# Kernel tuning notes

Measured on AMD Instinct MI355X. Metric: run time of the kernel, lower is better.

The kernel has to match this reference:

```python
import jax, jax.numpy as jnp
import numpy as np

BLOCK = 64
CRIT_TH = 0.5
NEGL_TH = 0.01
TEMP = 1.0
EPS = 1e-6


def setup_inputs() -> dict:
    key = jax.random.key(0)
    kq, kk, kv = jax.random.split(key, 3)
    B, T, H, D = 1, 2048, 8, 64
    q = jax.random.normal(kq, (B, T, H, D), dtype=jnp.float32)
    k = jax.random.normal(kk, (B, T, H, D), dtype=jnp.float32)
    v = jax.random.normal(kv, (B, T, H, D), dtype=jnp.float32)
    return {"q": q, "k": k, "v": v}


def _classify_blocks(qb, kb, D):
    # qb: [B,nq,bs,H,D], kb: [B,nk,bs,H,D]
    q_rep = qb.mean(axis=2)  # [B,nq,H,D]
    k_rep = kb.mean(axis=2)  # [B,nk,H,D]
    bscores = jnp.einsum('bqhd,bkhd->bhqk', q_rep, k_rep) / np.float32(np.sqrt(D))
    ssm = jax.nn.softmax(bscores, axis=-1)
    var = jnp.var(ssm, axis=-1, ddof=1, keepdims=True)  # unbiased, matches torch .var()
    max_scores = bscores.max(axis=-1, keepdims=True)
    imp = var * jnp.maximum(max_scores - bscores.min(), EPS)
    imp_n = (imp - imp.min()) / (imp.max() - imp.min() + EPS)
    crit = imp_n >= CRIT_TH
    negl = imp_n <= NEGL_TH
    marg = (~crit) & (~negl)
    return crit, marg


def reference(q, k, v):
    B, T, H, D = q.shape
    S = k.shape[1]
    nq, nk = T // BLOCK, S // BLOCK  # T,S are multiples of BLOCK (no padding needed)
    dtype = q.dtype

    qb = q.reshape(B, nq, BLOCK, H, D)
    kb = k.reshape(B, nk, BLOCK, H, D)
    vb = v.reshape(B, nk, BLOCK, H, D)

    crit, marg = _classify_blocks(qb, kb, D)  # [B,H,nq,nk] bool
    critf = crit.astype(dtype)
    margf = marg.astype(dtype)

    # ---- exact (critical) blocks: per-block-pair softmax attention ----
    scale = np.float32(1.0 / (np.sqrt(D) * TEMP))
    scores = jnp.einsum('bqthd,bkshd->bhqkts', qb, kb) * scale  # [B,H,nq,nk,bs,bs]
    attn = jax.nn.softmax(scores.astype(jnp.float32), axis=-1).astype(dtype)
    attn_m = attn * critf[:, :, :, :, None, None]
    out_c = jnp.einsum('bhqkts,bkshd->bqthd', attn_m, vb)  # [B,nq,bs,H,D]
    w_c = jnp.einsum('bhqkts->bqth', attn_m)[..., None]    # [B,nq,bs,H,1]

    # ---- linear (marginal) blocks: ELU+1 feature-map attention ----
    qf = jax.nn.elu(qb / TEMP) + 1.0
    kf = jax.nn.elu(kb / TEMP) + 1.0
    kv = jnp.einsum('bkshd,bkshv->bkhdv', kf, vb)              # [B,nk,H,D,D]
    num = jnp.einsum('bqthd,bkhdv->bqkthv', qf, kv)            # [B,nq,nk,bs,H,D]
    k_sum = kf.sum(axis=2)                                     # [B,nk,H,D]
    den = jnp.einsum('bqthd,bkhd->bqkth', qf, k_sum) + EPS     # [B,nq,nk,bs,H]
    out_pair = num / den[..., None]
    out_l = jnp.einsum('bqkthd,bhqk->bqthd', out_pair, margf)
    w_l = jnp.einsum('bqkth,bhqk->bqth', den, margf)[..., None]

    out = (out_c + out_l) / (w_c + w_l + EPS)
    return out.reshape(B, T, H, D)
```

## Files before the change

### kernel.cpp

```cpp
#include <hip/hip_runtime.h>
#include <math.h>

namespace {
constexpr int H  = 8;
constexpr int D  = 64;
constexpr int NB = 32;
constexpr int BS = 64;
constexpr int QST = 68;
}
#define FEPS 1e-6f

typedef unsigned short u16;
typedef unsigned int   u32;
typedef __attribute__((ext_vector_type(8))) short bf16x8;
typedef __attribute__((ext_vector_type(4))) float floatx4;

__device__ __forceinline__ u32 f2bf(float x) {
  union { float f; u32 u; } v; v.f = x;
  return (v.u + 0x7FFFu + ((v.u >> 16) & 1u)) >> 16;
}
__device__ __forceinline__ u32 pk2(float a, float b) { return f2bf(a) | (f2bf(b) << 16); }
#define ELU1(x) ((x) > 0.f ? (x) + 1.f : expf(x))
#define SWZ(row, kblk) ((row)*64 + (((kblk) ^ ((row)&7))*8))

__global__ __launch_bounds__(256) void prep_kernel(const float* __restrict__ q,
                                                   const float* __restrict__ k,
                                                   const float* __restrict__ v,
                                                   u16* __restrict__ kvt16,
                                                   float* __restrict__ ksum,
                                                   double* __restrict__ qrep,
                                                   double* __restrict__ krep) {
  __shared__ float smem[3*BS*D];
  int bid = blockIdx.x;
  int tid = threadIdx.x;
  if (bid >= 256) {
    double* qred = (double*)smem;
    int r = bid - 256;
    int h = r >> 5, bi = r & 31;
    int d = tid & 63, quarter = tid >> 6;
    double s = 0.0;
    for (int t = quarter*16; t < quarter*16 + 16; ++t)
      s += (double)q[((bi*BS + t)*H + h)*D + d];
    qred[quarter*64 + d] = s;
    __syncthreads();
    if (tid < 64)
      qrep[r*D + tid] = (qred[tid] + qred[64+tid] + qred[128+tid] + qred[192+tid]) * (1.0/64.0);
    return;
  }
  float* kf   = smem;
  float* vv   = smem + BS*D;
  float* kraw = smem + 2*BS*D;
  int h = bid >> 5, ki = bid & 31;
  int sr = tid >> 2, cgp = tid & 3;
  const float4* kb = (const float4*)(k + ((ki*BS + sr)*H + h)*D);
  const float4* vb = (const float4*)(v + ((ki*BS + sr)*H + h)*D);
#pragma unroll
  for (int m = 0; m < 4; ++m) {
    float4 kk = kb[cgp*4 + m];
    float4 vx = vb[cgp*4 + m];
    int c = cgp*16 + m*4;
    *(float4*)&kraw[sr*D + c] = kk;
    kf[sr*D + c + 0] = ELU1(kk.x);
    kf[sr*D + c + 1] = ELU1(kk.y);
    kf[sr*D + c + 2] = ELU1(kk.z);
    kf[sr*D + c + 3] = ELU1(kk.w);
    *(float4*)&vv[sr*D + c] = vx;
  }
  __syncthreads();
  int c = tid & 63, dg = tid >> 6, d0 = dg*16;
  float acc[16];
#pragma unroll
  for (int j = 0; j < 16; ++j) acc[j] = 0.f;
#pragma unroll 4
  for (int s2 = 0; s2 < BS; ++s2) {
    float vval = vv[s2*D + c];
    const float4* kr = (const float4*)&kf[s2*D + d0];
    float4 a0 = kr[0], a1 = kr[1], a2 = kr[2], a3 = kr[3];
    acc[0]  += vval*a0.x; acc[1]  += vval*a0.y; acc[2]  += vval*a0.z; acc[3]  += vval*a0.w;
    acc[4]  += vval*a1.x; acc[5]  += vval*a1.y; acc[6]  += vval*a1.z; acc[7]  += vval*a1.w;
    acc[8]  += vval*a2.x; acc[9]  += vval*a2.y; acc[10] += vval*a2.z; acc[11] += vval*a2.w;
    acc[12] += vval*a3.x; acc[13] += vval*a3.y; acc[14] += vval*a3.z; acc[15] += vval*a3.w;
  }
  u16* op = kvt16 + (size_t)bid*4096 + c*64 + d0;
  uint4 P0, P1;
  P0.x = pk2(acc[0],acc[1]);   P0.y = pk2(acc[2],acc[3]);
  P0.z = pk2(acc[4],acc[5]);   P0.w = pk2(acc[6],acc[7]);
  P1.x = pk2(acc[8],acc[9]);   P1.y = pk2(acc[10],acc[11]);
  P1.z = pk2(acc[12],acc[13]); P1.w = pk2(acc[14],acc[15]);
  *(uint4*)(op + 0) = P0;
  *(uint4*)(op + 8) = P1;
  if (dg == 0) {
    float ks = 0.f;
    for (int s2 = 0; s2 < BS; ++s2) ks += kf[s2*D + c];
    ksum[bid*D + c] = ks;
    double m = 0.0;
    for (int s2 = 0; s2 < BS; ++s2) m += (double)kraw[s2*D + c];
    krep[bid*D + c] = m * (1.0/64.0);
  }
}

__global__ __launch_bounds__(256) void bscore_stats_kernel(const double* __restrict__ qrep,
                                                           const double* __restrict__ krep,
                                                           double* __restrict__ rowmin,
                                                           double* __restrict__ rowmax,
                                                           double* __restrict__ rowvar) {
  __shared__ double qs[8*64];
  __shared__ double ks[32*65];
  int b = blockIdx.x;
  int h = b >> 2;
  int r0 = b*8;
  int tid = threadIdx.x;
  for (int i = tid; i < 512; i += 256) qs[i] = qrep[(size_t)r0*64 + i];
  for (int i = tid; i < 2048; i += 256) ks[(i >> 6)*65 + (i & 63)] = krep[(size_t)h*2048 + i];
  __syncthreads();
  int lr = tid >> 5, ki = tid & 31;
  double s = 0.0;
  const double* qr = qs + lr*64;
  const double* kr = ks + ki*65;
#pragma unroll 16
  for (int d = 0; d < D; ++d) s += qr[d]*kr[d];
  double bs = s * 0.125;
  double rmax = bs, rmin = bs;
#pragma unroll
  for (int m = 1; m < 32; m <<= 1) {
    rmax = fmax(rmax, __shfl_xor(rmax, m, 64));
    rmin = fmin(rmin, __shfl_xor(rmin, m, 64));
  }
  double e = exp(bs - rmax);
  double S = e, S2 = e*e;
#pragma unroll
  for (int m = 1; m < 32; m <<= 1) {
    S  += __shfl_xor(S,  m, 64);
    S2 += __shfl_xor(S2, m, 64);
  }
  if (ki == 0) {
    double invS = 1.0 / S;
    double sp = S * invS;
    double mu = sp * (1.0/32.0);
    double var = (S2*invS*invS - 2.0*mu*sp + 32.0*mu*mu) * (1.0/31.0);
    rowmin[r0 + lr] = rmin;
    rowmax[r0 + lr] = rmax;
    rowvar[r0 + lr] = var;
  }
}

__global__ __launch_bounds__(256) void main_kernel(
    const float* __restrict__ q, const float* __restrict__ k, const float* __restrict__ v,
    const u16* __restrict__ kvt16, const float* __restrict__ ksum,
    const double* __restrict__ rowmin, const double* __restrict__ rowmax,
    const double* __restrict__ rowvar, float* __restrict__ out) {
  __shared__ __align__(16) float smem[10304];
  int bid = blockIdx.x;
  int h = bid >> 5, qi = bid & 31;
  int tid = threadIdx.x;
  int row = tid >> 2, cgp = tid & 3, c0 = cgp*16;
  int lane = tid & 63;
  int wid = tid >> 6;

  int flag;
  {
    double* redA = (double*)smem;
    double* redB = (double*)(smem + 8);
    double* impS = (double*)(smem + 16);
    double x = rowmin[tid];
    double rmx2 = rowmax[tid];
    double rvr2 = rowvar[tid];
#pragma unroll
    for (int m = 1; m < 64; m <<= 1) x = fmin(x, __shfl_xor(x, m, 64));
    if (lane == 0) redA[wid] = x;
    __syncthreads();
    double gmin = fmin(fmin(redA[0], redA[1]), fmin(redA[2], redA[3]));
    double rng = rmx2 - gmin;
    if (rng < 1e-6) rng = 1e-6;
    double imp = rvr2 * rng;
    __syncthreads();
    if (tid == bid) impS[0] = imp;
    double a = imp, b2 = imp;
#pragma unroll
    for (int m = 1; m < 64; m <<= 1) {
      a  = fmin(a,  __shfl_xor(a,  m, 64));
      b2 = fmax(b2, __shfl_xor(b2, m, 64));
    }
    if (lane == 0) { redA[wid] = a; redB[wid] = b2; }
    __syncthreads();
    double imin = fmin(fmin(redA[0], redA[1]), fmin(redA[2], redA[3]));
    double imax = fmax(fmax(redB[0], redB[1]), fmax(redB[2], redB[3]));
    double impn = (impS[0] - imin) / (imax - imin + 1e-6);
    flag = (impn >= 0.5) ? 2 : ((impn <= 0.01) ? 0 : 1);
    __syncthreads();
  }

  if (flag == 1) {
    u16*  qfb  = (u16*)smem;
    u16*  kvb  = (u16*)(smem + 2048);
    float* idens = smem + 6144;
    float* wsl   = smem + 8192;
    float* kslc  = smem + 8256;

    {
      const float4* kss = (const float4*)(ksum + (size_t)(h*NB)*D);
      for (int i = tid; i < NB*16; i += 256) ((float4*)kslc)[i] = kss[i];
    }
    float qf[16];
    {
      const float4* qp = (const float4*)(q + ((qi*BS + row)*H + h)*D + c0);
      float4 q0 = qp[0], q1 = qp[1], q2 = qp[2], q3 = qp[3];
      qf[0]=ELU1(q0.x); qf[1]=ELU1(q0.y); qf[2]=ELU1(q0.z); qf[3]=ELU1(q0.w);
      qf[4]=ELU1(q1.x); qf[5]=ELU1(q1.y); qf[6]=ELU1(q1.z); qf[7]=ELU1(q1.w);
      qf[8]=ELU1(q2.x); qf[9]=ELU1(q2.y); qf[10]=ELU1(q2.z); qf[11]=ELU1(q2.w);
      qf[12]=ELU1(q3.x); qf[13]=ELU1(q3.y); qf[14]=ELU1(q3.z); qf[15]=ELU1(q3.w);
      uint4 p0, p1;
      p0.x = pk2(qf[0],qf[1]);  p0.y = pk2(qf[2],qf[3]);
      p0.z = pk2(qf[4],qf[5]);  p0.w = pk2(qf[6],qf[7]);
      p1.x = pk2(qf[8],qf[9]);  p1.y = pk2(qf[10],qf[11]);
      p1.z = pk2(qf[12],qf[13]); p1.w = pk2(qf[14],qf[15]);
      *(uint4*)&qfb[SWZ(row, cgp*2)]     = p0;
      *(uint4*)&qfb[SWZ(row, cgp*2 + 1)] = p1;
    }
    const u16* kvbase = kvt16 + (size_t)(h*NB)*4096 + (size_t)row*64 + c0;
    uint4 u0, u1;
    u0 = *(const uint4*)(kvbase + 0);
    u1 = *(const uint4*)(kvbase + 8);
    __syncthreads();
    {
      float wloc = 0.f;
      for (int ki = 0; ki < NB; ++ki) {
        float pd = 0.f;
#pragma unroll
        for (int j = 0; j < 16; ++j) pd += qf[j] * kslc[ki*64 + c0 + j];
        pd += __shfl_xor(pd, 1, 64);
        pd += __shfl_xor(pd, 2, 64);
        float den = pd + FEPS;
        if (cgp == 0) idens[row*32 + ki] = 1.0f / den;
        wloc += den;
      }
      if (cgp == 0) wsl[row] = wloc;
    }
    *(uint4*)&kvb[SWZ(row, cgp*2)]     = u0;
    *(uint4*)&kvb[SWZ(row, cgp*2 + 1)] = u1;

    int w = tid >> 6, m = lane & 15, quad = lane >> 4;
    bf16x8 aLo = *(const bf16x8*)&qfb[SWZ(w*16 + m, quad)];
    bf16x8 aHi = *(const bf16x8*)&qfb[SWZ(w*16 + m, 4 + quad)];
    int rbase = w*16 + quad*4;
    float acc[16];
#pragma unroll
    for (int j = 0; j < 16; ++j) acc[j] = 0.f;

    for (int ki = 0; ki < NB; ++ki) {
      if (ki + 1 < NB) {
        const u16* kvp = kvbase + (size_t)(ki+1)*4096;
        u0 = *(const uint4*)(kvp + 0);
        u1 = *(const uint4*)(kvp + 8);
      }
      __syncthreads();
      const u16* kb = kvb + (ki & 1)*4096;
      float i0 = idens[(rbase + 0)*32 + ki];
      float i1 = idens[(rbase + 1)*32 + ki];
      float i2 = idens[(rbase + 2)*32 + ki];
      float i3 = idens[(rbase + 3)*32 + ki];
      floatx4 zz = {0.f, 0.f, 0.f, 0.f};
#pragma unroll
      for (int t = 0; t < 4; ++t) {
        bf16x8 bLo = *(const bf16x8*)&kb[SWZ(t*16 + m, quad)];
        bf16x8 bHi = *(const bf16x8*)&kb[SWZ(t*16 + m, 4 + quad)];
        floatx4 c4 = __builtin_amdgcn_mfma_f32_16x16x32_bf16(aLo, bLo, zz, 0, 0, 0);
        c4 = __builtin_amdgcn_mfma_f32_16x16x32_bf16(aHi, bHi, c4, 0, 0, 0);
        acc[t*4+0] += c4[0]*i0;
        acc[t*4+1] += c4[1]*i1;
        acc[t*4+2] += c4[2]*i2;
        acc[t*4+3] += c4[3]*i3;
      }
      if (ki + 1 < NB) {
        u16* kw = kvb + ((ki+1) & 1)*4096;
        *(uint4*)&kw[SWZ(row, cgp*2)]     = u0;
        *(uint4*)&kw[SWZ(row, cgp*2 + 1)] = u1;
      }
    }
#pragma unroll
    for (int r = 0; r < 4; ++r) {
      float wd = 1.0f / (wsl[rbase + r] + FEPS);
      float* op = out + ((qi*BS + rbase + r)*H + h)*D + m;
#pragma unroll
      for (int t = 0; t < 4; ++t) op[t*16] = acc[t*4+r]*wd;
    }
    return;
  }

  float* bufA = smem;
  float* bufB = smem + 4352;
  float acc[16];
#pragma unroll
  for (int j = 0; j < 16; ++j) acc[j] = 0.f;
  float wsum = 0.f;

  if (flag == 2) {
    const float4* qp = (const float4*)(q + ((qi*BS + row)*H + h)*D);
#pragma unroll
    for (int mm = 0; mm < 4; ++mm) {
      float4 qq = qp[cgp*4 + mm];
      int c = c0 + mm*4;
      bufA[row*QST + c + 0] = qq.x*0.125f;
      bufA[row*QST + c + 1] = qq.y*0.125f;
      bufA[row*QST + c + 2] = qq.z*0.125f;
      bufA[row*QST + c + 3] = qq.w*0.125f;
    }
    __syncthreads();
    for (int ki = 0; ki < NB; ++ki) {
      const float4* kp = (const float4*)(k + ((ki*BS + row)*H + h)*D);
#pragma unroll
      for (int mm = 0; mm < 4; ++mm)
        *(float4*)&bufB[row*QST + c0 + mm*4] = kp[cgp*4 + mm];
      __syncthreads();
      float sc[16];
#pragma unroll
      for (int j = 0; j < 16; ++j) sc[j] = 0.f;
      for (int d = 0; d < D; ++d) {
        float a = bufA[row*QST + d];
#pragma unroll
        for (int j = 0; j < 16; ++j)
          sc[j] += a * bufB[(c0 + j)*QST + d];
      }
      float mx = sc[0];
#pragma unroll
      for (int j = 1; j < 16; ++j) mx = fmaxf(mx, sc[j]);
      mx = fmaxf(mx, __shfl_xor(mx, 1, 64));
      mx = fmaxf(mx, __shfl_xor(mx, 2, 64));
      float es = 0.f;
      float p[16];
#pragma unroll
      for (int j = 0; j < 16; ++j) { p[j] = expf(sc[j] - mx); es += p[j]; }
      es += __shfl_xor(es, 1, 64);
      es += __shfl_xor(es, 2, 64);
      float inv = 1.0f / es;
#pragma unroll
      for (int j = 0; j < 16; ++j) p[j] *= inv;
      wsum += es * inv;
      __syncthreads();
      const float4* vp = (const float4*)(v + ((ki*BS + row)*H + h)*D);
#pragma unroll
      for (int mm = 0; mm < 4; ++mm)
        *(float4*)&bufB[row*QST + c0 + mm*4] = vp[cgp*4 + mm];
      __syncthreads();
      for (int s2 = 0; s2 < BS; ++s2) {
        int g = s2 >> 4, jj = s2 & 15;
        float pv = __shfl(p[jj], (lane & ~3) | g, 64);
        const float4* vr = (const float4*)&bufB[s2*QST + c0];
        float4 a0 = vr[0], a1 = vr[1], a2 = vr[2], a3 = vr[3];
        acc[0]  += pv*a0.x; acc[1]  += pv*a0.y; acc[2]  += pv*a0.z; acc[3]  += pv*a0.w;
        acc[4]  += pv*a1.x; acc[5]  += pv*a1.y; acc[6]  += pv*a1.z; acc[7]  += pv*a1.w;
        acc[8]  += pv*a2.x; acc[9]  += pv*a2.y; acc[10] += pv*a2.z; acc[11] += pv*a2.w;
        acc[12] += pv*a3.x; acc[13] += pv*a3.y; acc[14] += pv*a3.z; acc[15] += pv*a3.w;
      }
      __syncthreads();
    }
  }
  float wd = 1.0f / (wsum + FEPS);
  float* op = out + ((qi*BS + row)*H + h)*D + c0;
  *(float4*)(op + 0)  = make_float4(acc[0]*wd,  acc[1]*wd,  acc[2]*wd,  acc[3]*wd);
  *(float4*)(op + 4)  = make_float4(acc[4]*wd,  acc[5]*wd,  acc[6]*wd,  acc[7]*wd);
  *(float4*)(op + 8)  = make_float4(acc[8]*wd,  acc[9]*wd,  acc[10]*wd, acc[11]*wd);
  *(float4*)(op + 12) = make_float4(acc[12]*wd, acc[13]*wd, acc[14]*wd, acc[15]*wd);
}

extern "C" void kernel_launch(void* const* d_in, const int* in_sizes, int n_in,
                              void* d_out, int out_size, void* d_ws, size_t ws_size,
                              hipStream_t stream) {
  const float* q = (const float*)d_in[0];
  const float* k = (const float*)d_in[1];
  const float* v = (const float*)d_in[2];
  float* out = (float*)d_out;
  char* ws = (char*)d_ws;
  u16*    kvw  = (u16*)   (ws + 0);
  float*  ksw  = (float*) (ws + 2097152);
  double* krep = (double*)(ws + 2162688);
  double* qrep = (double*)(ws + 2293760);
  double* rmn  = (double*)(ws + 2424832);
  double* rmx  = (double*)(ws + 2426880);
  double* rvr  = (double*)(ws + 2428928);

  prep_kernel<<<512, 256, 0, stream>>>(q, k, v, kvw, ksw, qrep, krep);
  bscore_stats_kernel<<<32, 256, 0, stream>>>(qrep, krep, rmn, rmx, rvr);
  main_kernel<<<256, 256, 0, stream>>>(q, k, v, kvw, ksw, rmn, rmx, rvr, out);
}
```

Measured before the change: 97.18 us.

## Split key-block loop across 8 workgroups with partial-sum combine kernel

The main attention kernel now splits the 32 key blocks of each (head, query-block) row over 8 workgroups. Each workgroup writes unnormalised partial accumulators and weights to workspace, and a new combine kernel sums and normalises them. Block classification moves into a separate single-block flags kernel, so it is no longer recomputed in every workgroup. The exact path also stores K transposed, prefetches K and V into registers, and vectorises its shared-memory loads. The goal is to raise occupancy from 256 workgroups and shorten the serial key loop. The cost is two extra launches and a large workspace round-trip for the partial results.

Result: slower. 103.5 us (+6.5%).

```diff
diff --git a/kernel.cpp b/kernel.cpp
--- a/kernel.cpp
+++ b/kernel.cpp
@@ -7,6 +7,8 @@
 constexpr int NB = 32;
 constexpr int BS = 64;
 constexpr int QST = 68;
+constexpr int KSPLIT = 8;
+constexpr int KCH = NB / KSPLIT;
 }
 #define FEPS 1e-6f
 
@@ -144,62 +146,71 @@
   }
 }
 
+__global__ __launch_bounds__(256) void flags_kernel(const double* __restrict__ rowmin,
+                                                    const double* __restrict__ rowmax,
+                                                    const double* __restrict__ rowvar,
+                                                    int* __restrict__ flags) {
+  __shared__ double redA[4];
+  __shared__ double redB[4];
+  int tid = threadIdx.x;
+  int lane = tid & 63, wid = tid >> 6;
+  double x = rowmin[tid];
+#pragma unroll
+  for (int m = 1; m < 64; m <<= 1) x = fmin(x, __shfl_xor(x, m, 64));
+  if (lane == 0) redA[wid] = x;
+  __syncthreads();
+  double gmin = fmin(fmin(redA[0], redA[1]), fmin(redA[2], redA[3]));
+  double rng = rowmax[tid] - gmin;
+  if (rng < 1e-6) rng = 1e-6;
+  double imp = rowvar[tid] * rng;
+  __syncthreads();
+  double a = imp, b2 = imp;
+#pragma unroll
+  for (int m = 1; m < 64; m <<= 1) {
+    a  = fmin(a,  __shfl_xor(a,  m, 64));
+    b2 = fmax(b2, __shfl_xor(b2, m, 64));
+  }
+  if (lane == 0) { redA[wid] = a; redB[wid] = b2; }
+  __syncthreads();
+  double imin = fmin(fmin(redA[0], redA[1]), fmin(redA[2], redA[3]));
+  double imax = fmax(fmax(redB[0], redB[1]), fmax(redB[2], redB[3]));
+  double impn = (imp - imin) / (imax - imin + 1e-6);
+  flags[tid] = (impn >= 0.5) ? 2 : ((impn <= 0.01) ? 0 : 1);
+}
+
 __global__ __launch_bounds__(256) void main_kernel(
     const float* __restrict__ q, const float* __restrict__ k, const float* __restrict__ v,
     const u16* __restrict__ kvt16, const float* __restrict__ ksum,
-    const double* __restrict__ rowmin, const double* __restrict__ rowmax,
-    const double* __restrict__ rowvar, float* __restrict__ out) {
-  __shared__ __align__(16) float smem[10304];
+    const int* __restrict__ flags, float* __restrict__ pacc, float* __restrict__ pw) {
+  __shared__ __align__(16) float smem[13056];
   int bid = blockIdx.x;
-  int h = bid >> 5, qi = bid & 31;
+  int rowid = bid >> 3;
+  int split = bid & (KSPLIT - 1);
+  int h = rowid >> 5, qi = rowid & 31;
+  int k0 = split * KCH;
   int tid = threadIdx.x;
   int row = tid >> 2, cgp = tid & 3, c0 = cgp*16;
   int lane = tid & 63;
-  int wid = tid >> 6;
-
-  int flag;
-  {
-    double* redA = (double*)smem;
-    double* redB = (double*)(smem + 8);
-    double* impS = (double*)(smem + 16);
-    double x = rowmin[tid];
-    double rmx2 = rowmax[tid];
-    double rvr2 = rowvar[tid];
-#pragma unroll
-    for (int m = 1; m < 64; m <<= 1) x = fmin(x, __shfl_xor(x, m, 64));
-    if (lane == 0) redA[wid] = x;
-    __syncthreads();
-    double gmin = fmin(fmin(redA[0], redA[1]), fmin(redA[2], redA[3]));
-    double rng = rmx2 - gmin;
-    if (rng < 1e-6) rng = 1e-6;
-    double imp = rvr2 * rng;
-    __syncthreads();
-    if (tid == bid) impS[0] = imp;
-    double a = imp, b2 = imp;
-#pragma unroll
-    for (int m = 1; m < 64; m <<= 1) {
-      a  = fmin(a,  __shfl_xor(a,  m, 64));
-      b2 = fmax(b2, __shfl_xor(b2, m, 64));
-    }
-    if (lane == 0) { redA[wid] = a; redB[wid] = b2; }
-    __syncthreads();
-    double imin = fmin(fmin(redA[0], redA[1]), fmin(redA[2], redA[3]));
-    double imax = fmax(fmax(redB[0], redB[1]), fmax(redB[2], redB[3]));
-    double impn = (impS[0] - imin) / (imax - imin + 1e-6);
-    flag = (impn >= 0.5) ? 2 : ((impn <= 0.01) ? 0 : 1);
-    __syncthreads();
+
+  float* paccp = pacc + (size_t)bid * 4096;
+  float* pwp   = pw   + (size_t)bid * 64;
+
+  int flag = flags[rowid];
+  if (flag == 0) {
+    if (tid < 64) pwp[tid] = 0.f;
+    return;
   }
 
   if (flag == 1) {
     u16*  qfb  = (u16*)smem;
     u16*  kvb  = (u16*)(smem + 2048);
     float* idens = smem + 6144;
-    float* wsl   = smem + 8192;
-    float* kslc  = smem + 8256;
+    float* wsl   = smem + 6400;
+    float* kslc  = smem + 6464;
 
     {
-      const float4* kss = (const float4*)(ksum + (size_t)(h*NB)*D);
-      for (int i = tid; i < NB*16; i += 256) ((float4*)kslc)[i] = kss[i];
+      const float4* kss = (const float4*)(ksum + (size_t)(h*NB + k0)*D);
+      for (int i = tid; i < KCH*16; i += 256) ((float4*)kslc)[i] = kss[i];
     }
     float qf[16];
     {
@@ -217,21 +228,20 @@
       *(uint4*)&qfb[SWZ(row, cgp*2)]     = p0;
       *(uint4*)&qfb[SWZ(row, cgp*2 + 1)] = p1;
     }
-    const u16* kvbase = kvt16 + (size_t)(h*NB)*4096 + (size_t)row*64 + c0;
-    uint4 u0, u1;
-    u0 = *(const uint4*)(kvbase + 0);
-    u1 = *(const uint4*)(kvbase + 8);
+    const u16* kvbase = kvt16 + (size_t)(h*NB + k0)*4096 + (size_t)row*64 + c0;
+    uint4 u0 = *(const uint4*)(kvbase + 0);
+    uint4 u1 = *(const uint4*)(kvbase + 8);
     __syncthreads();
     {
       float wloc = 0.f;
-      for (int ki = 0; ki < NB; ++ki) {
+      for (int kk = 0; kk < KCH; ++kk) {
         float pd = 0.f;
 #pragma unroll
-        for (int j = 0; j < 16; ++j) pd += qf[j] * kslc[ki*64 + c0 + j];
+        for (int j = 0; j < 16; ++j) pd += qf[j] * kslc[kk*64 + c0 + j];
         pd += __shfl_xor(pd, 1, 64);
         pd += __shfl_xor(pd, 2, 64);
         float den = pd + FEPS;
-        if (cgp == 0) idens[row*32 + ki] = 1.0f / den;
+        if (cgp == 0) idens[row*KCH + kk] = 1.0f / den;
         wloc += den;
       }
       if (cgp == 0) wsl[row] = wloc;
@@ -247,18 +257,18 @@
 #pragma unroll
     for (int j = 0; j < 16; ++j) acc[j] = 0.f;
 
-    for (int ki = 0; ki < NB; ++ki) {
-      if (ki + 1 < NB) {
-        const u16* kvp = kvbase + (size_t)(ki+1)*4096;
+    for (int kk = 0; kk < KCH; ++kk) {
+      if (kk + 1 < KCH) {
+        const u16* kvp = kvbase + (size_t)(kk+1)*4096;
         u0 = *(const uint4*)(kvp + 0);
         u1 = *(const uint4*)(kvp + 8);
       }
       __syncthreads();
-      const u16* kb = kvb + (ki & 1)*4096;
-      float i0 = idens[(rbase + 0)*32 + ki];
-      float i1 = idens[(rbase + 1)*32 + ki];
-      float i2 = idens[(rbase + 2)*32 + ki];
-      float i3 = idens[(rbase + 3)*32 + ki];
+      const u16* kb = kvb + (kk & 1)*4096;
+      float i0 = idens[(rbase + 0)*KCH + kk];
+      float i1 = idens[(rbase + 1)*KCH + kk];
+      float i2 = idens[(rbase + 2)*KCH + kk];
+      float i3 = idens[(rbase + 3)*KCH + kk];
       floatx4 zz = {0.f, 0.f, 0.f, 0.f};
 #pragma unroll
       for (int t = 0; t < 4; ++t) {
@@ -271,30 +281,25 @@
         acc[t*4+2] += c4[2]*i2;
         acc[t*4+3] += c4[3]*i3;
       }
-      if (ki + 1 < NB) {
-        u16* kw = kvb + ((ki+1) & 1)*4096;
+      if (kk + 1 < KCH) {
+        u16* kw = kvb + ((kk+1) & 1)*4096;
         *(uint4*)&kw[SWZ(row, cgp*2)]     = u0;
         *(uint4*)&kw[SWZ(row, cgp*2 + 1)] = u1;
       }
     }
 #pragma unroll
-    for (int r = 0; r < 4; ++r) {
-      float wd = 1.0f / (wsl[rbase + r] + FEPS);
-      float* op = out + ((qi*BS + rbase + r)*H + h)*D + m;
-#pragma unroll
-      for (int t = 0; t < 4; ++t) op[t*16] = acc[t*4+r]*wd;
-    }
+    for (int r = 0; r < 4; ++r)
+#pragma unroll
+      for (int t = 0; t < 4; ++t)
+        paccp[(rbase + r)*64 + t*16 + m] = acc[t*4 + r];
+    if (tid < 64) pwp[tid] = wsl[tid];
     return;
   }
 
   float* bufA = smem;
-  float* bufB = smem + 4352;
-  float acc[16];
-#pragma unroll
-  for (int j = 0; j < 16; ++j) acc[j] = 0.f;
-  float wsum = 0.f;
-
-  if (flag == 2) {
+  float* bufK = smem + 4352;
+  float* bufV = smem + 8704;
+  {
     const float4* qp = (const float4*)(q + ((qi*BS + row)*H + h)*D);
 #pragma unroll
     for (int mm = 0; mm < 4; ++mm) {
@@ -305,62 +310,124 @@
       bufA[row*QST + c + 2] = qq.z*0.125f;
       bufA[row*QST + c + 3] = qq.w*0.125f;
     }
+  }
+  float4 kreg[4], vreg[4];
+  {
+    const float4* kp = (const float4*)(k + ((k0*BS + row)*H + h)*D);
+    const float4* vp = (const float4*)(v + ((k0*BS + row)*H + h)*D);
+#pragma unroll
+    for (int mm = 0; mm < 4; ++mm) { kreg[mm] = kp[cgp*4 + mm]; vreg[mm] = vp[cgp*4 + mm]; }
+  }
+  float acc[16];
+#pragma unroll
+  for (int j = 0; j < 16; ++j) acc[j] = 0.f;
+  float wsum = 0.f;
+
+#pragma unroll 1
+  for (int kk = 0; kk < KCH; ++kk) {
+#pragma unroll
+    for (int mm = 0; mm < 4; ++mm) {
+      int c = c0 + mm*4;
+      bufK[(c+0)*QST + row] = kreg[mm].x;
+      bufK[(c+1)*QST + row] = kreg[mm].y;
+      bufK[(c+2)*QST + row] = kreg[mm].z;
+      bufK[(c+3)*QST + row] = kreg[mm].w;
+      *(float4*)&bufV[row*QST + c] = vreg[mm];
+    }
     __syncthreads();
-    for (int ki = 0; ki < NB; ++ki) {
-      const float4* kp = (const float4*)(k + ((ki*BS + row)*H + h)*D);
-#pragma unroll
-      for (int mm = 0; mm < 4; ++mm)
-        *(float4*)&bufB[row*QST + c0 + mm*4] = kp[cgp*4 + mm];
-      __syncthreads();
-      float sc[16];
-#pragma unroll
-      for (int j = 0; j < 16; ++j) sc[j] = 0.f;
-      for (int d = 0; d < D; ++d) {
-        float a = bufA[row*QST + d];
-#pragma unroll
-        for (int j = 0; j < 16; ++j)
-          sc[j] += a * bufB[(c0 + j)*QST + d];
-      }
-      float mx = sc[0];
-#pragma unroll
-      for (int j = 1; j < 16; ++j) mx = fmaxf(mx, sc[j]);
-      mx = fmaxf(mx, __shfl_xor(mx, 1, 64));
-      mx = fmaxf(mx, __shfl_xor(mx, 2, 64));
-      float es = 0.f;
-      float p[16];
-#pragma unroll
-      for (int j = 0; j < 16; ++j) { p[j] = expf(sc[j] - mx); es += p[j]; }
-      es += __shfl_xor(es, 1, 64);
-      es += __shfl_xor(es, 2, 64);
-      float inv = 1.0f / es;
-#pragma unroll
-      for (int j = 0; j < 16; ++j) p[j] *= inv;
-      wsum += es * inv;
-      __syncthreads();
-      const float4* vp = (const float4*)(v + ((ki*BS + row)*H + h)*D);
-#pragma unroll
-      for (int mm = 0; mm < 4; ++mm)
-        *(float4*)&bufB[row*QST + c0 + mm*4] = vp[cgp*4 + mm];
-      __syncthreads();
-      for (int s2 = 0; s2 < BS; ++s2) {
-        int g = s2 >> 4, jj = s2 & 15;
-        float pv = __shfl(p[jj], (lane & ~3) | g, 64);
-        const float4* vr = (const float4*)&bufB[s2*QST + c0];
+    if (kk + 1 < KCH) {
+      int ki1 = k0 + kk + 1;
+      const float4* kp = (const float4*)(k + ((ki1*BS + row)*H + h)*D);
+      const float4* vp = (const float4*)(v + ((ki1*BS + row)*H + h)*D);
+#pragma unroll
+      for (int mm = 0; mm < 4; ++mm) { kreg[mm] = kp[cgp*4 + mm]; vreg[mm] = vp[cgp*4 + mm]; }
+    }
+    float sc[16];
+#pragma unroll
+    for (int j = 0; j < 16; ++j) sc[j] = 0.f;
+#pragma unroll 4
+    for (int d4 = 0; d4 < 16; ++d4) {
+      float4 a4 = *(const float4*)&bufA[row*QST + d4*4];
+      float av[4] = {a4.x, a4.y, a4.z, a4.w};
+#pragma unroll
+      for (int x = 0; x < 4; ++x) {
+        const float4* br = (const float4*)&bufK[(d4*4 + x)*QST + c0];
+        float4 b0 = br[0], b1 = br[1], b2 = br[2], b3 = br[3];
+        float a = av[x];
+        sc[0]  += a*b0.x; sc[1]  += a*b0.y; sc[2]  += a*b0.z; sc[3]  += a*b0.w;
+        sc[4]  += a*b1.x; sc[5]  += a*b1.y; sc[6]  += a*b1.z; sc[7]  += a*b1.w;
+        sc[8]  += a*b2.x; sc[9]  += a*b2.y; sc[10] += a*b2.z; sc[11] += a*b2.w;
+        sc[12] += a*b3.x; sc[13] += a*b3.y; sc[14] += a*b3.z; sc[15] += a*b3.w;
+      }
+    }
+    float mx = sc[0];
+#pragma unroll
+    for (int j = 1; j < 16; ++j) mx = fmaxf(mx, sc[j]);
+    mx = fmaxf(mx, __shfl_xor(mx, 1, 64));
+    mx = fmaxf(mx, __shfl_xor(mx, 2, 64));
+    float es = 0.f;
+    float p[16];
+#pragma unroll
+    for (int j = 0; j < 16; ++j) { p[j] = expf(sc[j] - mx); es += p[j]; }
+    es += __shfl_xor(es, 1, 64);
+    es += __shfl_xor(es, 2, 64);
+    float inv = 1.0f / es;
+#pragma unroll
+    for (int j = 0; j < 16; ++j) p[j] *= inv;
+    wsum += es * inv;
+#pragma unroll 1
+    for (int g = 0; g < 4; ++g) {
+      int src = (lane & ~3) | g;
+#pragma unroll
+      for (int jj = 0; jj < 16; ++jj) {
+        float pv = __shfl(p[jj], src, 64);
+        const float4* vr = (const float4*)&bufV[(g*16 + jj)*QST + c0];
         float4 a0 = vr[0], a1 = vr[1], a2 = vr[2], a3 = vr[3];
         acc[0]  += pv*a0.x; acc[1]  += pv*a0.y; acc[2]  += pv*a0.z; acc[3]  += pv*a0.w;
         acc[4]  += pv*a1.x; acc[5]  += pv*a1.y; acc[6]  += pv*a1.z; acc[7]  += pv*a1.w;
         acc[8]  += pv*a2.x; acc[9]  += pv*a2.y; acc[10] += pv*a2.z; acc[11] += pv*a2.w;
         acc[12] += pv*a3.x; acc[13] += pv*a3.y; acc[14] += pv*a3.z; acc[15] += pv*a3.w;
       }
-      __syncthreads();
-    }
-  }
-  float wd = 1.0f / (wsum + FEPS);
+    }
+    __syncthreads();
+  }
+  float* pp = paccp + row*64 + c0;
+  *(float4*)(pp + 0)  = make_float4(acc[0],  acc[1],  acc[2],  acc[3]);
+  *(float4*)(pp + 4)  = make_float4(acc[4],  acc[5],  acc[6],  acc[7]);
+  *(float4*)(pp + 8)  = make_float4(acc[8],  acc[9],  acc[10], acc[11]);
+  *(float4*)(pp + 12) = make_float4(acc[12], acc[13], acc[14], acc[15]);
+  if (cgp == 0) pwp[row] = wsum;
+}
+
+__global__ __launch_bounds__(256) void combine_kernel(const float* __restrict__ pacc,
+                                                      const float* __restrict__ pw,
+                                                      float* __restrict__ out) {
+  int rowid = blockIdx.x;
+  int h = rowid >> 5, qi = rowid & 31;
+  int tid = threadIdx.x;
+  int row = tid >> 2, c0 = (tid & 3)*16;
+  float w = 0.f;
+  const float* pwb = pw + (size_t)rowid * KSPLIT * 64 + row;
+#pragma unroll
+  for (int s = 0; s < KSPLIT; ++s) w += pwb[s*64];
   float* op = out + ((qi*BS + row)*H + h)*D + c0;
-  *(float4*)(op + 0)  = make_float4(acc[0]*wd,  acc[1]*wd,  acc[2]*wd,  acc[3]*wd);
-  *(float4*)(op + 4)  = make_float4(acc[4]*wd,  acc[5]*wd,  acc[6]*wd,  acc[7]*wd);
-  *(float4*)(op + 8)  = make_float4(acc[8]*wd,  acc[9]*wd,  acc[10]*wd, acc[11]*wd);
-  *(float4*)(op + 12) = make_float4(acc[12]*wd, acc[13]*wd, acc[14]*wd, acc[15]*wd);
+  if (w == 0.f) {
+    float4 z = make_float4(0.f, 0.f, 0.f, 0.f);
+    ((float4*)op)[0] = z; ((float4*)op)[1] = z; ((float4*)op)[2] = z; ((float4*)op)[3] = z;
+    return;
+  }
+  floatx4 s0 = {0,0,0,0}, s1 = {0,0,0,0}, s2 = {0,0,0,0}, s3 = {0,0,0,0};
+  const float* base = pacc + (size_t)rowid * KSPLIT * 4096 + row*64 + c0;
+#pragma unroll
+  for (int s = 0; s < KSPLIT; ++s) {
+    const floatx4* p4 = (const floatx4*)(base + (size_t)s*4096);
+    s0 += p4[0]; s1 += p4[1]; s2 += p4[2]; s3 += p4[3];
+  }
+  float wd = 1.0f / (w + FEPS);
+  ((float4*)op)[0] = make_float4(s0[0]*wd, s0[1]*wd, s0[2]*wd, s0[3]*wd);
+  ((float4*)op)[1] = make_float4(s1[0]*wd, s1[1]*wd, s1[2]*wd, s1[3]*wd);
+  ((float4*)op)[2] = make_float4(s2[0]*wd, s2[1]*wd, s2[2]*wd, s2[3]*wd);
+  ((float4*)op)[3] = make_float4(s3[0]*wd, s3[1]*wd, s3[2]*wd, s3[3]*wd);
 }
 
 extern "C" void kernel_launch(void* const* d_in, const int* in_sizes, int n_in,
@@ -378,8 +445,13 @@
   double* rmn  = (double*)(ws + 2424832);
   double* rmx  = (double*)(ws + 2426880);
   double* rvr  = (double*)(ws + 2428928);
+  int*    flg  = (int*)   (ws + 2430976);
+  float*  pacc = (float*) (ws + 4194304);
+  float*  pw   = (float*) (ws + 4194304 + 33554432);
 
   prep_kernel<<<512, 256, 0, stream>>>(q, k, v, kvw, ksw, qrep, krep);
   bscore_stats_kernel<<<32, 256, 0, stream>>>(qrep, krep, rmn, rmx, rvr);
-  main_kernel<<<256, 256, 0, stream>>>(q, k, v, kvw, ksw, rmn, rmx, rvr, out);
-}
+  flags_kernel<<<1, 256, 0, stream>>>(rmn, rmx, rvr, flg);
+  main_kernel<<<256*KSPLIT, 256, 0, stream>>>(q, k, v, kvw, ksw, flg, pacc, pw);
+  combine_kernel<<<256, 256, 0, stream>>>(pacc, pw, out);
+}
```
